# Optimization experiments

Measured on AMD Instinct MI355X. Metric: run time of the kernel, lower is better.

The kernel has to match this reference:

```python
import jax, jax.numpy as jnp
import numpy as np

NUM_EMBEDDINGS = 1024
EMBEDDING_DIM = 256


def setup_inputs() -> dict:
    key = jax.random.key(0)
    kx, kw = jax.random.split(key)
    x = jax.random.normal(kx, (64, 32, 32, EMBEDDING_DIM), dtype=jnp.float32)
    # nn.Linear(embedding_dim, num_embeddings).weight has shape [K, D]
    W = jax.random.normal(kw, (NUM_EMBEDDINGS, EMBEDDING_DIM), dtype=jnp.float32) * (1.0 / np.sqrt(EMBEDDING_DIM))
    return {"x": x, "W": W}


def reference(x, W):
    # flatten tokens: [N, D]
    flat = x.reshape(-1, EMBEDDING_DIM)
    sim = flat @ W.T
    distances = (jnp.sum(flat * flat, axis=1, keepdims=True)
                 + jnp.sum(W * W, axis=1)
                 - 2.0 * sim)
    indices = jnp.argmin(distances, axis=1)[:, None]  # [N, 1], matches torch unsqueeze(1)
    # one-hot @ W is exactly a row gather of the codebook
    quantized = jnp.take(W, indices[:, 0], axis=0).reshape(x.shape)
    return quantized, indices
```

## Files before the change

kernel.cpp:

```cpp
#include <hip/hip_runtime.h>
#include <float.h>

typedef int i32x16 __attribute__((ext_vector_type(16)));

#define NTOK  65536
#define DIM   256
#define NCODE 1024
#define TT    128
#define NCT   16
#define CAP   4096
#define TAU   0.35f
#define BIAS  64.0f
#define SX    20.0f
#define SW    360.0f

__device__ inline unsigned q4(float4 v, float s) {
    int q0 = (int)rintf(fminf(fmaxf(v.x * s, -127.f), 127.f));
    int q1 = (int)rintf(fminf(fmaxf(v.y * s, -127.f), 127.f));
    int q2 = (int)rintf(fminf(fmaxf(v.z * s, -127.f), 127.f));
    int q3 = (int)rintf(fminf(fmaxf(v.w * s, -127.f), 127.f));
    return (unsigned)(q0 & 255) | ((unsigned)(q1 & 255) << 8) |
           ((unsigned)(q2 & 255) << 16) | ((unsigned)(q3 & 255) << 24);
}
__device__ inline long pk8(float4 a, float4 b, float s) {
    union { unsigned u[2]; long l; } r;
    r.u[0] = q4(a, s); r.u[1] = q4(b, s);
    return r.l;
}
__device__ inline unsigned umn(unsigned a, unsigned b) { return a < b ? a : b; }
__device__ inline unsigned umx(unsigned a, unsigned b) { return a > b ? a : b; }

__device__ inline void gload16(const void* g, void* l) {
    __builtin_amdgcn_global_load_lds(
        (__attribute__((address_space(1))) void*)(size_t)g,
        (__attribute__((address_space(3))) void*)l,
        16, 0, 0);
}

__global__ __launch_bounds__(256) void prep_kernel(const float* __restrict__ W,
                                                   float* __restrict__ nw_out,
                                                   long* __restrict__ wq_out) {
    const int tid = threadIdx.x;
    const int k = blockIdx.x * 8 + (tid >> 5);
    const int c = tid & 31;
    const float4* wr = (const float4*)(W + (size_t)k * DIM + c * 8);
    float4 u = wr[0], v = wr[1];
    wq_out[(size_t)k * 32 + c] = pk8(u, v, SW);
    double a = (double)u.x * u.x + (double)u.y * u.y + (double)u.z * u.z + (double)u.w * u.w
             + (double)v.x * v.x + (double)v.y * v.y + (double)v.z * v.z + (double)v.w * v.w;
    #pragma unroll
    for (int m = 1; m <= 16; m <<= 1) a += __shfl_xor(a, m);
    if (c == 0) nw_out[k] = (float)a;
}

template <bool PRE>
__global__ __launch_bounds__(256, 2)
void vq_kernel(
    const float* __restrict__ x, const float* __restrict__ W,
    const float* __restrict__ nwp, const long* __restrict__ wqp,
    float* __restrict__ outq, float* __restrict__ outidx)
{
    __shared__ __align__(16) char wtile[64][256];
    __shared__ float nw_s[NCODE];
    __shared__ float nx_s[TT];
    __shared__ unsigned long long best64[TT];
    __shared__ int cnt_s;
    __shared__ int bk_s[TT];
    unsigned* cand = (unsigned*)&wtile[0][0];

    const int tid = threadIdx.x, tb = blockIdx.x * TT;
    const int wv = tid >> 6, l = tid & 63;
    const int ln = l & 31;
    const int h = l >> 5;

    if (PRE) {
        ((float4*)nw_s)[tid] = ((const float4*)nwp)[tid];
    } else {
        #pragma unroll
        for (int c = 0; c < 4; ++c) {
            const int k = (tid << 2) + c;
            const float4* wr = (const float4*)(W + (size_t)k * DIM);
            double a0 = 0.0, a1 = 0.0;
            for (int q = 0; q < DIM / 4; ++q) {
                float4 v = wr[q];
                a0 += (double)v.x * v.x + (double)v.y * v.y;
                a1 += (double)v.z * v.z + (double)v.w * v.w;
            }
            nw_s[k] = (float)(a0 + a1);
        }
    }
    if (tid == 0) cnt_s = 0;
    if (tid < TT) best64[tid] = ~0ull;

    const int trow = tb + (wv << 5) + ln;
    long xa[16];
    {
        const float4* xr = (const float4*)(x + (size_t)trow * DIM);
        double a0 = 0.0, a1 = 0.0;
        #pragma unroll
        for (int sp = 0; sp < 16; ++sp) {
            float4 u = xr[(sp << 2) + (h << 1)];
            float4 v = xr[(sp << 2) + (h << 1) + 1];
            xa[sp] = pk8(u, v, SX);
            a0 += (double)u.x * u.x + (double)u.y * u.y + (double)v.x * v.x + (double)v.y * v.y;
            a1 += (double)u.z * u.z + (double)u.w * u.w + (double)v.z * v.z + (double)v.w * v.w;
        }
        double nx = a0 + a1;
        nx += __shfl_xor(nx, 32);
        if (h == 0) nx_s[(wv << 5) + ln] = (float)nx;
    }

    unsigned b0[16], b1[16];
    #pragma unroll
    for (int j = 0; j < 16; ++j) { b0[j] = 0xFFFFFFFFu; b1[j] = 0xFFFFFFFFu; }

    const float M2 = -2.0f / (SX * SW);

    for (int ct = 0; ct < NCT; ++ct) {
        __syncthreads();
        if (PRE) {
            #pragma unroll
            for (int j = 0; j < 4; ++j) {
                const unsigned C = (unsigned)(j * 256 + tid);
                const unsigned src = (C & ~15u) | ((C & 15u) ^ ((C >> 4) & 15u));
                gload16((const char*)wqp + (size_t)ct * 16384 + (size_t)src * 16,
                        &wtile[0][0] + (size_t)C * 16);
            }
        } else {
            const int n = tid >> 2, qq = tid & 3;
            const float4* srcp = (const float4*)(W + (size_t)(ct * 64 + n) * DIM);
            #pragma unroll
            for (int i = 0; i < 4; ++i) {
                const int c16 = (qq << 2) + i;
                float4 f0 = srcp[c16 * 4 + 0], f1 = srcp[c16 * 4 + 1];
                float4 f2 = srcp[c16 * 4 + 2], f3 = srcp[c16 * 4 + 3];
                long* dst = (long*)(&wtile[n][0] + ((c16 ^ (n & 15)) << 4));
                dst[0] = pk8(f0, f1, SW);
                dst[1] = pk8(f2, f3, SW);
            }
        }
        __syncthreads();

        i32x16 a0, a1;
        #pragma unroll
        for (int j = 0; j < 16; ++j) { a0[j] = 0; a1[j] = 0; }

        #pragma unroll
        for (int sp = 0; sp < 16; ++sp) {
            const int gr = (sp << 1) + h;
            const int swz = gr ^ ((ln & 15) << 1);
            const char* p0 = &wtile[0][0] + ln * 256 + (swz << 3);
            long bq0 = *(const long*)p0;
            long bq1 = *(const long*)(p0 + 8192);
            a0 = __builtin_amdgcn_mfma_i32_32x32x16_i8(xa[sp], bq0, a0, 0, 0, 0);
            a1 = __builtin_amdgcn_mfma_i32_32x32x16_i8(xa[sp], bq1, a1, 0, 0, 0);
        }

        const int kk0 = (ct << 6) + ln;
        const int kk1 = kk0 + 32;
        const float nwb0 = nw_s[kk0] + BIAS;
        const float nwb1 = nw_s[kk1] + BIAS;
        #pragma unroll
        for (int j = 0; j < 16; ++j) {
            const float c0 = fmaf((float)a0[j], M2, nwb0);
            unsigned u = (__float_as_uint(c0) & 0xFFFFFC00u) | (unsigned)kk0;
            unsigned lo = umn(u, b0[j]), hi = umx(u, b0[j]);
            b0[j] = lo; b1[j] = umn(hi, b1[j]);
            const float c1 = fmaf((float)a1[j], M2, nwb1);
            u = (__float_as_uint(c1) & 0xFFFFFC00u) | (unsigned)kk1;
            lo = umn(u, b0[j]); hi = umx(u, b0[j]);
            b0[j] = lo; b1[j] = umn(hi, b1[j]);
        }
    }

    __syncthreads();

    #pragma unroll
    for (int j = 0; j < 16; ++j) {
        unsigned v = b0[j];
        #pragma unroll
        for (int m = 1; m <= 16; m <<= 1) v = umn(v, (unsigned)__shfl_xor((int)v, m));
        const float thr = __uint_as_float(v & 0xFFFFFC00u) + TAU;
        const int t = (wv << 5) + (j & 3) + ((j >> 2) << 3) + (h << 2);
        if (__uint_as_float(b0[j] & 0xFFFFFC00u) <= thr) {
            int i = atomicAdd(&cnt_s, 1);
            if (i < CAP) cand[i] = ((unsigned)t << 10) | (b0[j] & 1023u);
        }
        if (__uint_as_float(b1[j] & 0xFFFFFC00u) <= thr) {
            int i = atomicAdd(&cnt_s, 1);
            if (i < CAP) cand[i] = ((unsigned)t << 10) | (b1[j] & 1023u);
        }
    }
    __syncthreads();

    const int nc = min(cnt_s, CAP);
    for (int c = wv; c < nc; c += 4) {
        const unsigned en = cand[c];
        const int t = en >> 10, k = en & 1023;
        float4 xv = ((const float4*)(x + (size_t)(tb + t) * DIM))[l];
        float4 wr = ((const float4*)(W + (size_t)k * DIM))[l];
        float s = fmaf(xv.x, wr.x, fmaf(xv.y, wr.y, fmaf(xv.z, wr.z, xv.w * wr.w)));
        #pragma unroll
        for (int m = 1; m <= 32; m <<= 1) s += __shfl_xor(s, m);
        const float dv = (nx_s[t] + nw_s[k]) - 2.0f * s;
        if (l == 0) {
            unsigned long long key = ((unsigned long long)__float_as_uint(dv) << 32) | (unsigned)k;
            atomicMin(&best64[t], key);
        }
    }
    __syncthreads();

    if (tid < TT) {
        const int bk = (int)(best64[tid] & 1023u);
        bk_s[tid] = bk;
        outidx[tb + tid] = (float)bk;
    }
    __syncthreads();

    for (int i = tid; i < TT * (DIM / 4); i += 256) {
        const int t = i >> 6, j = i & 63;
        const float4* wr = (const float4*)(W + (size_t)bk_s[t] * DIM);
        ((float4*)(outq + (size_t)(tb + t) * DIM))[j] = wr[j];
    }
}

extern "C" void kernel_launch(void* const* d_in, const int* in_sizes, int n_in,
                              void* d_out, int out_size, void* d_ws, size_t ws_size,
                              hipStream_t stream) {
    const float* x = (const float*)d_in[0];
    const float* W = (const float*)d_in[1];
    float* outq   = (float*)d_out;
    float* outidx = outq + (size_t)NTOK * DIM;

    const size_t need = 4096 + (size_t)NCODE * DIM;
    if (ws_size >= need) {
        float* nw_ws = (float*)d_ws;
        long* wq_ws = (long*)((char*)d_ws + 4096);
        prep_kernel<<<NCODE / 8, 256, 0, stream>>>(W, nw_ws, wq_ws);
        vq_kernel<true><<<NTOK / TT, 256, 0, stream>>>(x, W, nw_ws, wq_ws, outq, outidx);
    } else {
        vq_kernel<false><<<NTOK / TT, 256, 0, stream>>>(x, W, nullptr, nullptr, outq, outidx);
    }
}
```

Measured before the change: 179.2 us.

## Halve token tile and split codebook columns across waves with shared min threshold

Token tile per block drops from 128 to 64, and the four waves become two token groups times two codebook halves. Each wave now runs one MFMA accumulator instead of two, and per-token minima from the two column halves are merged through an LDS atomicMin before candidate filtering. The prepacked codebook layout switches to a column-major 8-byte-group layout, so the LDS swizzle is no longer needed. This doubles the block count for more parallelism and lowers register pressure, but each block now reloads the full codebook for half as many tokens.

```diff
diff --git a/kernel.cpp b/kernel.cpp
--- a/kernel.cpp
+++ b/kernel.cpp
@@ -6,7 +6,7 @@
 #define NTOK  65536
 #define DIM   256
 #define NCODE 1024
-#define TT    128
+#define TT    64
 #define NCT   16
 #define CAP   4096
 #define TAU   0.35f
@@ -45,7 +45,7 @@
     const int c = tid & 31;
     const float4* wr = (const float4*)(W + (size_t)k * DIM + c * 8);
     float4 u = wr[0], v = wr[1];
-    wq_out[(size_t)k * 32 + c] = pk8(u, v, SW);
+    wq_out[(size_t)(k >> 6) * 2048 + (size_t)c * 64 + (k & 63)] = pk8(u, v, SW);
     double a = (double)u.x * u.x + (double)u.y * u.y + (double)u.z * u.z + (double)u.w * u.w
              + (double)v.x * v.x + (double)v.y * v.y + (double)v.z * v.z + (double)v.w * v.w;
     #pragma unroll
@@ -60,18 +60,21 @@
     const float* __restrict__ nwp, const long* __restrict__ wqp,
     float* __restrict__ outq, float* __restrict__ outidx)
 {
-    __shared__ __align__(16) char wtile[64][256];
+    __shared__ __align__(16) char wtile[16384];
     __shared__ float nw_s[NCODE];
     __shared__ float nx_s[TT];
+    __shared__ unsigned tmin_s[TT];
     __shared__ unsigned long long best64[TT];
     __shared__ int cnt_s;
     __shared__ int bk_s[TT];
-    unsigned* cand = (unsigned*)&wtile[0][0];
+    unsigned* cand = (unsigned*)wtile;
 
     const int tid = threadIdx.x, tb = blockIdx.x * TT;
     const int wv = tid >> 6, l = tid & 63;
     const int ln = l & 31;
     const int h = l >> 5;
+    const int tg = wv & 1;
+    const int cg = wv >> 1;
 
     if (PRE) {
         ((float4*)nw_s)[tid] = ((const float4*)nwp)[tid];
@@ -90,9 +93,9 @@
         }
     }
     if (tid == 0) cnt_s = 0;
-    if (tid < TT) best64[tid] = ~0ull;
-
-    const int trow = tb + (wv << 5) + ln;
+    if (tid < TT) { best64[tid] = ~0ull; tmin_s[tid] = 0xFFFFFFFFu; }
+
+    const int trow = tb + (tg << 5) + ln;
     long xa[16];
     {
         const float4* xr = (const float4*)(x + (size_t)trow * DIM);
@@ -102,12 +105,16 @@
             float4 u = xr[(sp << 2) + (h << 1)];
             float4 v = xr[(sp << 2) + (h << 1) + 1];
             xa[sp] = pk8(u, v, SX);
-            a0 += (double)u.x * u.x + (double)u.y * u.y + (double)v.x * v.x + (double)v.y * v.y;
-            a1 += (double)u.z * u.z + (double)u.w * u.w + (double)v.z * v.z + (double)v.w * v.w;
-        }
-        double nx = a0 + a1;
-        nx += __shfl_xor(nx, 32);
-        if (h == 0) nx_s[(wv << 5) + ln] = (float)nx;
+            if (cg == 0) {
+                a0 += (double)u.x * u.x + (double)u.y * u.y + (double)v.x * v.x + (double)v.y * v.y;
+                a1 += (double)u.z * u.z + (double)u.w * u.w + (double)v.z * v.z + (double)v.w * v.w;
+            }
+        }
+        if (cg == 0) {
+            double nx = a0 + a1;
+            nx += __shfl_xor(nx, 32);
+            if (h == 0) nx_s[(tg << 5) + ln] = (float)nx;
+        }
     }
 
     unsigned b0[16], b1[16];
@@ -121,67 +128,60 @@
         if (PRE) {
             #pragma unroll
             for (int j = 0; j < 4; ++j) {
-                const unsigned C = (unsigned)(j * 256 + tid);
-                const unsigned src = (C & ~15u) | ((C & 15u) ^ ((C >> 4) & 15u));
-                gload16((const char*)wqp + (size_t)ct * 16384 + (size_t)src * 16,
-                        &wtile[0][0] + (size_t)C * 16);
+                const int C = j * 256 + tid;
+                gload16((const char*)wqp + (size_t)ct * 16384 + (size_t)C * 16,
+                        wtile + (size_t)C * 16);
             }
         } else {
-            const int n = tid >> 2, qq = tid & 3;
-            const float4* srcp = (const float4*)(W + (size_t)(ct * 64 + n) * DIM);
+            const int n = tid >> 2, q = tid & 3;
+            const float4* srcp = (const float4*)(W + (size_t)(ct * 64 + n) * DIM + (q << 6));
             #pragma unroll
-            for (int i = 0; i < 4; ++i) {
-                const int c16 = (qq << 2) + i;
-                float4 f0 = srcp[c16 * 4 + 0], f1 = srcp[c16 * 4 + 1];
-                float4 f2 = srcp[c16 * 4 + 2], f3 = srcp[c16 * 4 + 3];
-                long* dst = (long*)(&wtile[n][0] + ((c16 ^ (n & 15)) << 4));
-                dst[0] = pk8(f0, f1, SW);
-                dst[1] = pk8(f2, f3, SW);
+            for (int i = 0; i < 8; ++i) {
+                float4 f0 = srcp[2 * i], f1 = srcp[2 * i + 1];
+                const int g = (q << 3) + i;
+                *(long*)(wtile + ((size_t)(g << 6) + n) * 8) = pk8(f0, f1, SW);
             }
         }
         __syncthreads();
 
-        i32x16 a0, a1;
-        #pragma unroll
-        for (int j = 0; j < 16; ++j) { a0[j] = 0; a1[j] = 0; }
-
+        i32x16 acc;
+        #pragma unroll
+        for (int j = 0; j < 16; ++j) acc[j] = 0;
+
+        const char* bp = wtile + (h << 9) + (cg << 8) + (ln << 3);
         #pragma unroll
         for (int sp = 0; sp < 16; ++sp) {
-            const int gr = (sp << 1) + h;
-            const int swz = gr ^ ((ln & 15) << 1);
-            const char* p0 = &wtile[0][0] + ln * 256 + (swz << 3);
-            long bq0 = *(const long*)p0;
-            long bq1 = *(const long*)(p0 + 8192);
-            a0 = __builtin_amdgcn_mfma_i32_32x32x16_i8(xa[sp], bq0, a0, 0, 0, 0);
-            a1 = __builtin_amdgcn_mfma_i32_32x32x16_i8(xa[sp], bq1, a1, 0, 0, 0);
-        }
-
-        const int kk0 = (ct << 6) + ln;
-        const int kk1 = kk0 + 32;
-        const float nwb0 = nw_s[kk0] + BIAS;
-        const float nwb1 = nw_s[kk1] + BIAS;
+            long bq = *(const long*)(bp + (sp << 10));
+            acc = __builtin_amdgcn_mfma_i32_32x32x16_i8(xa[sp], bq, acc, 0, 0, 0);
+        }
+
+        const int kk = (ct << 6) + (cg << 5) + ln;
+        const float nwb = nw_s[kk] + BIAS;
         #pragma unroll
         for (int j = 0; j < 16; ++j) {
-            const float c0 = fmaf((float)a0[j], M2, nwb0);
-            unsigned u = (__float_as_uint(c0) & 0xFFFFFC00u) | (unsigned)kk0;
-            unsigned lo = umn(u, b0[j]), hi = umx(u, b0[j]);
+            const float cs = fmaf((float)acc[j], M2, nwb);
+            const unsigned u = (__float_as_uint(cs) & 0xFFFFFC00u) | (unsigned)kk;
+            const unsigned lo = umn(u, b0[j]), hi = umx(u, b0[j]);
             b0[j] = lo; b1[j] = umn(hi, b1[j]);
-            const float c1 = fmaf((float)a1[j], M2, nwb1);
-            u = (__float_as_uint(c1) & 0xFFFFFC00u) | (unsigned)kk1;
-            lo = umn(u, b0[j]); hi = umx(u, b0[j]);
-            b0[j] = lo; b1[j] = umn(hi, b1[j]);
-        }
-    }
-
-    __syncthreads();
+        }
+    }
 
     #pragma unroll
     for (int j = 0; j < 16; ++j) {
         unsigned v = b0[j];
         #pragma unroll
         for (int m = 1; m <= 16; m <<= 1) v = umn(v, (unsigned)__shfl_xor((int)v, m));
-        const float thr = __uint_as_float(v & 0xFFFFFC00u) + TAU;
-        const int t = (wv << 5) + (j & 3) + ((j >> 2) << 3) + (h << 2);
+        if (ln == 0) {
+            const int t = (tg << 5) + (j & 3) + ((j >> 2) << 3) + (h << 2);
+            atomicMin(&tmin_s[t], v & 0xFFFFFC00u);
+        }
+    }
+    __syncthreads();
+
+    #pragma unroll
+    for (int j = 0; j < 16; ++j) {
+        const int t = (tg << 5) + (j & 3) + ((j >> 2) << 3) + (h << 2);
+        const float thr = __uint_as_float(tmin_s[t]) + TAU;
         if (__uint_as_float(b0[j] & 0xFFFFFC00u) <= thr) {
             int i = atomicAdd(&cnt_s, 1);
             if (i < CAP) cand[i] = ((unsigned)t << 10) | (b0[j] & 1023u);
```

Measured after the change: 207.4 us. 1.16x slower.
